# Optimization experiments

Measured on AMD Instinct MI355X. Metric: run time of the kernel, lower is better.

## Reference

```python
import jax, jax.numpy as jnp
import numpy as np

N, E = 100000, 1600000
D_IN, D_H, D_OUT = 128, 128, 64


def _lin(key, fan_in, fan_out):
    return jax.random.normal(key, (fan_out, fan_in), jnp.float32) / np.sqrt(fan_in).astype(np.float32)


def setup_inputs() -> dict:
    key = jax.random.key(0)
    ks = jax.random.split(key, 12)
    x = jax.random.normal(ks[0], (N, D_IN), jnp.float32)
    edge_index = jax.random.randint(ks[1], (2, E), 0, N, dtype=jnp.int64)
    inp = {
        "x": x,
        "edge_index": edge_index,
        "emb_W": _lin(ks[2], D_IN, D_H),
        "emb_b": jnp.zeros((D_H,), jnp.float32),
        # SAGEConv layer 0 (hidden -> hidden): lin_l (on aggregated msgs, with bias), lin_r (root, no bias)
        "Wl0": _lin(ks[3], D_H, D_H), "bl0": jnp.zeros((D_H,), jnp.float32), "Wr0": _lin(ks[4], D_H, D_H),
        # SAGEConv layer 1 (hidden -> hidden)
        "Wl1": _lin(ks[5], D_H, D_H), "bl1": jnp.zeros((D_H,), jnp.float32), "Wr1": _lin(ks[6], D_H, D_H),
        # SAGEConv layer 2 (hidden -> out)
        "Wl2": _lin(ks[7], D_H, D_OUT), "bl2": jnp.zeros((D_OUT,), jnp.float32), "Wr2": _lin(ks[8], D_H, D_OUT),
    }
    return inp


def _sage_conv(h, src, dst, Wl, bl, Wr):
    # mean aggregation of source-node messages at destination nodes
    msg = h[src]                                               # [E, H] gather
    agg = jax.ops.segment_sum(msg, dst, num_segments=N)        # [N, H]
    cnt = jax.ops.segment_sum(jnp.ones((src.shape[0], 1), h.dtype), dst, num_segments=N)
    mean = agg / jnp.maximum(cnt, 1.0)
    return mean @ Wl.T + bl + h @ Wr.T


def reference(x, edge_index, emb_W, emb_b, Wl0, bl0, Wr0, Wl1, bl1, Wr1, Wl2, bl2, Wr2):
    src, dst = edge_index[0], edge_index[1]
    h = x @ emb_W.T + emb_b                                    # node_embedding Linear
    h = jax.nn.relu(_sage_conv(h, src, dst, Wl0, bl0, Wr0))    # dropout = identity (eval)
    h = jax.nn.relu(_sage_conv(h, src, dst, Wl1, bl1, Wr1))
    h = _sage_conv(h, src, dst, Wl2, bl2, Wr2)                 # final layer: no relu/dropout
    return h
```

## Files before the change

### kernel.cpp

```cpp
#include <hip/hip_runtime.h>

typedef __attribute__((ext_vector_type(8))) short short8;
typedef __attribute__((ext_vector_type(4))) float f32x4;
typedef __attribute__((ext_vector_type(2))) float f32x2;

#define NODE_D 128
#define ECH 16384
#define PSH 9

__device__ __forceinline__ float bf2f(ushort u) {
    union { uint i; float f; } c; c.i = ((uint)u) << 16; return c.f;
}
__device__ __forceinline__ ushort f2bf(float f) {
    union { float f; uint i; } c; c.f = f;
    return (ushort)((c.i + 0x7FFF + ((c.i >> 16) & 1)) >> 16);
}
__device__ __forceinline__ uchar f2e4m3(float f) {
    uint w = (uint)__builtin_amdgcn_cvt_pk_fp8_f32(f, f, 0, false);
    return (uchar)(w & 0xff);
}

__global__ __launch_bounds__(256) void k_count(const int* __restrict__ dst,
                                               int* __restrict__ cm,
                                               int E, int NC,
                                               const float* __restrict__ s0, const float* __restrict__ s1,
                                               const float* __restrict__ s2, const float* __restrict__ s3,
                                               const float* __restrict__ s4, const float* __restrict__ s5,
                                               const float* __restrict__ s6, ushort* __restrict__ wdst) {
    if ((int)blockIdx.x >= NC) {
        int i = ((int)blockIdx.x - NC) * 256 + threadIdx.x;
        if (i >= 98304) return;
        const float* s; int off;
        if (i < 16384)      { s = s0; off = i; }
        else if (i < 32768) { s = s1; off = i - 16384; }
        else if (i < 49152) { s = s2; off = i - 32768; }
        else if (i < 65536) { s = s3; off = i - 49152; }
        else if (i < 81920) { s = s4; off = i - 65536; }
        else if (i < 90112) { s = s5; off = i - 81920; }
        else                { s = s6; off = i - 90112; }
        wdst[i] = f2bf(s[off]);
        return;
    }
    __shared__ int lh[256];
    lh[threadIdx.x] = 0;
    __syncthreads();
    int c = blockIdx.x;
    int lo = c * ECH, hi = min(lo + ECH, E);
    for (int i = lo + (int)threadIdx.x; i < hi; i += 256)
        atomicAdd(&lh[dst[i] >> PSH], 1);
    __syncthreads();
    cm[c * 256 + threadIdx.x] = lh[threadIdx.x];
}

__global__ __launch_bounds__(256) void k_pscan(const int* __restrict__ cm,
                                               int* __restrict__ om,
                                               int* __restrict__ pbase,
                                               int* __restrict__ rowptrN,
                                               int NC, int NP, int E) {
    __shared__ int ts[256];
    int p = threadIdx.x;
    int s = 0;
    if (p < NP)
        for (int c = 0; c < NC; ++c) s += cm[c * 256 + p];
    ts[p] = s;
    __syncthreads();
    for (int st = 1; st < 256; st <<= 1) {
        int add = (p >= st) ? ts[p - st] : 0;
        __syncthreads();
        ts[p] += add;
        __syncthreads();
    }
    int base = ts[p] - s;
    if (p < NP) {
        int run = base;
        for (int c = 0; c < NC; ++c) {
            om[c * 256 + p] = run;
            run += cm[c * 256 + p];
        }
        pbase[p] = base;
    }
    if (p == 0) { pbase[NP] = E; rowptrN[0] = E; }
}

__global__ __launch_bounds__(256) void k_scatter3(const int* __restrict__ src,
                                                  const int* __restrict__ dst,
                                                  const int* __restrict__ om,
                                                  uint* __restrict__ ebuf, int E) {
    __shared__ int cur[256];
    int c = blockIdx.x;
    cur[threadIdx.x] = om[c * 256 + threadIdx.x];
    __syncthreads();
    int lo = c * ECH, hi = min(lo + ECH, E);
    for (int i = lo + (int)threadIdx.x; i < hi; i += 256) {
        int d = dst[i];
        int pos = atomicAdd(&cur[d >> PSH], 1);
        ebuf[pos] = ((uint)(d & 511) << 17) | (uint)src[i];
    }
}

__global__ __launch_bounds__(256) void k_local(const uint* __restrict__ ebuf,
                                               const int* __restrict__ pbase,
                                               int* __restrict__ rowptr,
                                               int* __restrict__ col, int N) {
    __shared__ int hist[512];
    __shared__ int cur[512];
    __shared__ int ts[256];
    int p = blockIdx.x;
    int t = threadIdx.x;
    int lo = pbase[p], hi = pbase[p + 1];
    hist[t] = 0; hist[t + 256] = 0;
    __syncthreads();
    for (int j = lo + t; j < hi; j += 256)
        atomicAdd(&hist[ebuf[j] >> 17], 1);
    __syncthreads();
    int v0 = hist[2 * t], v1 = hist[2 * t + 1];
    int s = v0 + v1;
    ts[t] = s;
    __syncthreads();
    for (int st = 1; st < 256; st <<= 1) {
        int add = (t >= st) ? ts[t - st] : 0;
        __syncthreads();
        ts[t] += add;
        __syncthreads();
    }
    int excl = ts[t] - s + lo;
    int node0 = (p << PSH) + 2 * t;
    if (node0 < N) rowptr[node0] = excl;
    if (node0 + 1 < N) rowptr[node0 + 1] = excl + v0;
    cur[2 * t] = excl;
    cur[2 * t + 1] = excl + v0;
    __syncthreads();
    for (int j = lo + t; j < hi; j += 256) {
        uint e = ebuf[j];
        int pos = atomicAdd(&cur[e >> 17], 1);
        col[pos] = (int)(e & 0x1FFFF);
    }
}

__global__ __launch_bounds__(256) void k_aggf(const uchar* __restrict__ hq,
                                              const int* __restrict__ rowptr,
                                              const int* __restrict__ col,
                                              ushort* __restrict__ mean, int N) {
    int node = blockIdx.x * 4 + (threadIdx.x >> 6);
    if (node >= N) return;
    int lane = threadIdx.x & 63;
    int half = lane >> 5;
    int l32  = lane & 31;
    int beg = rowptr[node];
    int end = rowptr[node + 1];
    float inv = 1.f / fmaxf((float)(end - beg), 1.f);
    const uchar* base = hq + l32 * 4;
    float a0 = 0.f, a1 = 0.f, a2 = 0.f, a3 = 0.f;
    for (int jb0 = beg; jb0 < end; jb0 += 16) {
        int bj = jb0 + half * 8;
        uint v[8];
        float mk[8];
        #pragma unroll
        for (int q = 0; q < 8; ++q) {
            int j = bj + q;
            int s = col[j < end ? j : end - 1];
            v[q] = *(const uint*)(base + (size_t)s * 128);
            mk[q] = (j < end) ? 1.f : 0.f;
        }
        #pragma unroll
        for (int q = 0; q < 8; ++q) {
            f32x2 lo = __builtin_amdgcn_cvt_pk_f32_fp8(v[q], false);
            f32x2 hi = __builtin_amdgcn_cvt_pk_f32_fp8(v[q], true);
            a0 += mk[q] * lo[0]; a1 += mk[q] * lo[1];
            a2 += mk[q] * hi[0]; a3 += mk[q] * hi[1];
        }
    }
    a0 += __shfl_xor(a0, 32); a1 += __shfl_xor(a1, 32);
    a2 += __shfl_xor(a2, 32); a3 += __shfl_xor(a3, 32);
    if (half == 0) {
        uint2 o;
        o.x = (uint)f2bf(a0 * inv) | ((uint)f2bf(a1 * inv) << 16);
        o.y = (uint)f2bf(a2 * inv) | ((uint)f2bf(a3 * inv) << 16);
        *(uint2*)(mean + (size_t)node * 128 + l32 * 4) = o;
    }
}

template<int OD, bool DUAL, bool RELU, int OMODE, bool A0F32>
__global__ __launch_bounds__(256) void k_mm(const void* __restrict__ A0,
                                            const ushort* __restrict__ A1,
                                            const ushort* __restrict__ W0,
                                            const ushort* __restrict__ W1,
                                            const float* __restrict__ bias,
                                            void* __restrict__ outp,
                                            uchar* __restrict__ f8out, int N) {
    constexpr int NK    = DUAL ? 4 : 2;
    constexpr int M_REP = (OD == 128) ? 4 : 2;
    constexpr int N_REP = 4;
    constexpr int WROWS = M_REP * 16;

    __shared__ __align__(16) ushort sA[128 * 64];
    __shared__ __align__(16) ushort sW[OD * 64];

    const int t    = threadIdx.x;
    const int wid  = t >> 6;
    const int lane = t & 63;
    const int l15  = lane & 15;
    const int lhi  = lane >> 4;
    const int r0   = blockIdx.x * 128;

    int wm, wn0;
    if (OD == 128) { wm = wid >> 1; wn0 = (wid & 1) * 64; }
    else           { wm = wid;      wn0 = 0; }

    f32x4 zero = {0.f, 0.f, 0.f, 0.f};
    f32x4 acc[M_REP][N_REP];
    #pragma unroll
    for (int m = 0; m < M_REP; ++m)
        #pragma unroll
        for (int n = 0; n < N_REP; ++n) acc[m][n] = zero;

    const ushort* A0b = (const ushort*)A0;
    const float*  A0f = (const float*)A0;

    for (int kc = 0; kc < NK; ++kc) {
        const ushort* Ws = (DUAL && kc >= 2) ? W1 : W0;
        const ushort* As = (DUAL && kc >= 2) ? A1 : A0b;
        const int kloc = (kc & 1) * 64;

        __syncthreads();
        #pragma unroll
        for (int it = 0; it < 4; ++it) {
            int slot = it * 256 + t;
            int row = slot >> 3, k8 = slot & 7;
            int gr = r0 + row; if (gr >= N) gr = N - 1;
            short8 v;
            if (A0F32 && kc < 2) {
                float4 p = *(const float4*)(A0f + (size_t)gr * 128 + kloc + k8 * 8);
                float4 q = *(const float4*)(A0f + (size_t)gr * 128 + kloc + k8 * 8 + 4);
                v[0] = (short)f2bf(p.x); v[1] = (short)f2bf(p.y);
                v[2] = (short)f2bf(p.z); v[3] = (short)f2bf(p.w);
                v[4] = (short)f2bf(q.x); v[5] = (short)f2bf(q.y);
                v[6] = (short)f2bf(q.z); v[7] = (short)f2bf(q.w);
            } else {
                v = *(const short8*)(As + (size_t)gr * 128 + kloc + k8 * 8);
            }
            *(short8*)((char*)sA + ((row * 128 + k8 * 16) ^ ((row & 7) << 4))) = v;
        }
        #pragma unroll
        for (int it = 0; it < OD / 32; ++it) {
            int slot = it * 256 + t;
            int row = slot >> 3, k8 = slot & 7;
            short8 v = *(const short8*)(Ws + (size_t)row * 128 + kloc + k8 * 8);
            *(short8*)((char*)sW + ((row * 128 + k8 * 16) ^ ((row & 7) << 4))) = v;
        }
        __syncthreads();

        #pragma unroll
        for (int kb = 0; kb < 2; ++kb) {
            short8 af[M_REP], bfr[N_REP];
            #pragma unroll
            for (int m = 0; m < M_REP; ++m) {
                int row = wm * WROWS + m * 16 + l15;
                af[m] = *(const short8*)((const char*)sA +
                        ((row * 128 + kb * 64 + lhi * 16) ^ ((row & 7) << 4)));
            }
            #pragma unroll
            for (int n = 0; n < N_REP; ++n) {
                int colr = wn0 + n * 16 + l15;
                bfr[n] = *(const short8*)((const char*)sW +
                         ((colr * 128 + kb * 64 + lhi * 16) ^ ((colr & 7) << 4)));
            }
            #pragma unroll
            for (int m = 0; m < M_REP; ++m)
                #pragma unroll
                for (int n = 0; n < N_REP; ++n)
                    acc[m][n] = __builtin_amdgcn_mfma_f32_16x16x32_bf16(af[m], bfr[n], acc[m][n], 0, 0, 0);
        }
    }

    float bv[N_REP];
    #pragma unroll
    for (int n = 0; n < N_REP; ++n) bv[n] = bias ? bias[wn0 + n * 16 + l15] : 0.f;

    #pragma unroll
    for (int m = 0; m < M_REP; ++m) {
        #pragma unroll
        for (int r = 0; r < 4; ++r) {
            int grow = r0 + wm * WROWS + m * 16 + lhi * 4 + r;
            if (grow < N) {
                #pragma unroll
                for (int n = 0; n < N_REP; ++n) {
                    int colr = wn0 + n * 16 + l15;
                    float v = acc[m][n][r] + bv[n];
                    if (RELU) v = fmaxf(v, 0.f);
                    if constexpr (OMODE != 3)
                        ((ushort*)outp)[(size_t)grow * OD + colr] = f2bf(v);
                    if constexpr (OMODE == 2 || OMODE == 3)
                        f8out[(size_t)grow * OD + colr] = f2e4m3(v);
                }
            }
        }
    }
}

__global__ __launch_bounds__(256) void k_fin(const uchar* __restrict__ gq,
                                             const ushort* __restrict__ h_in,
                                             const ushort* __restrict__ W0,
                                             const float* __restrict__ bias,
                                             const int* __restrict__ rowptr,
                                             const int* __restrict__ col,
                                             float* __restrict__ outp, int N) {
    __shared__ __align__(16) ushort ga[128 * 64];
    __shared__ __align__(16) ushort sA[128 * 64];
    __shared__ __align__(16) ushort sW[64 * 64];

    const int t    = threadIdx.x;
    const int wid  = t >> 6;
    const int lane = t & 63;
    const int g    = lane >> 4;
    const int c16  = lane & 15;
    const int r0   = blockIdx.x * 128;

    for (int it = 0; it < 8; ++it) {
        int nl = it * 16 + wid * 4 + g;
        int node = r0 + nl;
        float a0 = 0.f, a1 = 0.f, a2 = 0.f, a3 = 0.f;
        if (node < N) {
            int beg = rowptr[node], end = rowptr[node + 1];
            float inv = 1.f / fmaxf((float)(end - beg), 1.f);
            const uchar* base = gq + c16 * 4;
            for (int jb0 = beg; jb0 < end; jb0 += 8) {
                uint v[8];
                float mk[8];
                #pragma unroll
                for (int q = 0; q < 8; ++q) {
                    int j = jb0 + q;
                    int s = col[j < end ? j : end - 1];
                    v[q] = *(const uint*)(base + (size_t)s * 64);
                    mk[q] = (j < end) ? 1.f : 0.f;
                }
                #pragma unroll
                for (int q = 0; q < 8; ++q) {
                    f32x2 lo = __builtin_amdgcn_cvt_pk_f32_fp8(v[q], false);
                    f32x2 hi = __builtin_amdgcn_cvt_pk_f32_fp8(v[q], true);
                    a0 += mk[q] * lo[0]; a1 += mk[q] * lo[1];
                    a2 += mk[q] * hi[0]; a3 += mk[q] * hi[1];
                }
            }
            a0 *= inv; a1 *= inv; a2 *= inv; a3 *= inv;
        }
        uint2 o;
        o.x = (uint)f2bf(a0) | ((uint)f2bf(a1) << 16);
        o.y = (uint)f2bf(a2) | ((uint)f2bf(a3) << 16);
        *(uint2*)((char*)ga + nl * 128 + c16 * 8) = o;
    }

    const int l15 = lane & 15;
    const int lhi = lane >> 4;

    f32x4 zero = {0.f, 0.f, 0.f, 0.f};
    f32x4 acc[2][4];
    #pragma unroll
    for (int m = 0; m < 2; ++m)
        #pragma unroll
        for (int n = 0; n < 4; ++n) acc[m][n] = zero;

    for (int kc = 0; kc < 2; ++kc) {
        const int kloc = kc * 64;
        __syncthreads();
        #pragma unroll
        for (int it = 0; it < 4; ++it) {
            int slot = it * 256 + t;
            int row = slot >> 3, k8 = slot & 7;
            int gr = r0 + row; if (gr >= N) gr = N - 1;
            short8 v = *(const short8*)(h_in + (size_t)gr * 128 + kloc + k8 * 8);
            *(short8*)((char*)sA + ((row * 128 + k8 * 16) ^ ((row & 7) << 4))) = v;
        }
        #pragma unroll
        for (int it = 0; it < 2; ++it) {
            int slot = it * 256 + t;
            int row = slot >> 3, k8 = slot & 7;
            short8 v = *(const short8*)(W0 + (size_t)row * 128 + kloc + k8 * 8);
            *(short8*)((char*)sW + ((row * 128 + k8 * 16) ^ ((row & 7) << 4))) = v;
        }
        __syncthreads();

        #pragma unroll
        for (int kb = 0; kb < 2; ++kb) {
            short8 af[2], bfr[4];
            #pragma unroll
            for (int m = 0; m < 2; ++m) {
                int row = wid * 32 + m * 16 + l15;
                af[m] = *(const short8*)((const char*)sA +
                        ((row * 128 + kb * 64 + lhi * 16) ^ ((row & 7) << 4)));
            }
            #pragma unroll
            for (int n = 0; n < 4; ++n) {
                int colr = n * 16 + l15;
                bfr[n] = *(const short8*)((const char*)sW +
                         ((colr * 128 + kb * 64 + lhi * 16) ^ ((colr & 7) << 4)));
            }
            #pragma unroll
            for (int m = 0; m < 2; ++m)
                #pragma unroll
                for (int n = 0; n < 4; ++n)
                    acc[m][n] = __builtin_amdgcn_mfma_f32_16x16x32_bf16(af[m], bfr[n], acc[m][n], 0, 0, 0);
        }
    }

    float bv[4];
    #pragma unroll
    for (int n = 0; n < 4; ++n) bv[n] = bias[n * 16 + l15];

    #pragma unroll
    for (int m = 0; m < 2; ++m) {
        #pragma unroll
        for (int r = 0; r < 4; ++r) {
            int rl = wid * 32 + m * 16 + lhi * 4 + r;
            int grow = r0 + rl;
            if (grow < N) {
                #pragma unroll
                for (int n = 0; n < 4; ++n) {
                    int colr = n * 16 + l15;
                    float v = acc[m][n][r] + bv[n] + bf2f(ga[rl * 64 + colr]);
                    outp[(size_t)grow * 64 + colr] = v;
                }
            }
        }
    }
}

extern "C" void kernel_launch(void* const* d_in, const int* in_sizes, int n_in,
                              void* d_out, int out_size, void* d_ws, size_t ws_size,
                              hipStream_t stream) {
    const float* x     = (const float*)d_in[0];
    const int*   eidx  = (const int*)d_in[1];
    const float* emb_W = (const float*)d_in[2];
    const float* emb_b = (const float*)d_in[3];
    const float* Wl0   = (const float*)d_in[4];
    const float* bl0   = (const float*)d_in[5];
    const float* Wr0   = (const float*)d_in[6];
    const float* Wl1   = (const float*)d_in[7];
    const float* bl1   = (const float*)d_in[8];
    const float* Wr1   = (const float*)d_in[9];
    const float* Wl2   = (const float*)d_in[10];
    const float* bl2   = (const float*)d_in[11];
    const float* Wr2   = (const float*)d_in[12];

    const int N = in_sizes[0] / NODE_D;
    const int E = in_sizes[1] / 2;
    const int* src = eidx;
    const int* dst = eidx + E;
    const int NC = (E + ECH - 1) / ECH;
    const int NP = (N + (1 << PSH) - 1) >> PSH;

    char* w = (char*)d_ws;
    ushort* h_bf    = (ushort*)w; w += (size_t)N * 128 * sizeof(ushort);
    ushort* mean_bf = (ushort*)w; w += (size_t)N * 128 * sizeof(ushort);
    ushort* wbf     = (ushort*)w; w += (size_t)98304 * sizeof(ushort);
    uchar* q8_a     = (uchar*)w;  w += (size_t)N * 128;
    uchar* q8_b     = (uchar*)w;  w += (size_t)N * 128;
    uint* ebuf      = (uint*)w;   w += (size_t)E * sizeof(uint);
    int* cm     = (int*)w; w += (size_t)NC * 256 * sizeof(int);
    int* om     = (int*)w; w += (size_t)NC * 256 * sizeof(int);
    int* pbase  = (int*)w; w += (size_t)(NP + 1) * sizeof(int);
    int* rowptr = (int*)w; w += (size_t)(N + 1) * sizeof(int);
    int* col    = (int*)w; w += (size_t)E * sizeof(int);

    uchar* g2_q8 = (uchar*)mean_bf;

    const ushort* embB = wbf;
    const ushort* Wl0B = wbf + 16384;
    const ushort* Wr0B = wbf + 32768;
    const ushort* Wl1B = wbf + 49152;
    const ushort* Wr1B = wbf + 65536;
    const ushort* Wl2B = wbf + 81920;
    const ushort* Wr2B = wbf + 90112;

    const int TPB = 256;

    hipLaunchKernelGGL(k_count, dim3(NC + 384), dim3(TPB), 0, stream,
                       dst, cm, E, NC, emb_W, Wl0, Wr0, Wl1, Wr1, Wl2, Wr2, wbf);
    hipLaunchKernelGGL(k_pscan, dim3(1), dim3(TPB), 0, stream,
                       cm, om, pbase, rowptr + N, NC, NP, E);
    hipLaunchKernelGGL(k_scatter3, dim3(NC), dim3(TPB), 0, stream, src, dst, om, ebuf, E);
    hipLaunchKernelGGL(k_local, dim3(NP), dim3(TPB), 0, stream, ebuf, pbase, rowptr, col, N);

    const int dgrid = (N + 127) / 128;
    const int agrid = (N + 3) / 4;

    hipLaunchKernelGGL((k_mm<128, false, false, 2, true>), dim3(dgrid), dim3(TPB), 0, stream,
                       (const void*)x, (const ushort*)nullptr, embB, (const ushort*)nullptr,
                       emb_b, h_bf, q8_a, N);

    hipLaunchKernelGGL(k_aggf, dim3(agrid), dim3(TPB), 0, stream, q8_a, rowptr, col, mean_bf, N);
    hipLaunchKernelGGL((k_mm<128, true, true, 2, false>), dim3(dgrid), dim3(TPB), 0, stream,
                       (const void*)mean_bf, h_bf, Wl0B, Wr0B, bl0, h_bf, q8_b, N);

    hipLaunchKernelGGL(k_aggf, dim3(agrid), dim3(TPB), 0, stream, q8_b, rowptr, col, mean_bf, N);
    hipLaunchKernelGGL((k_mm<128, true, true, 0, false>), dim3(dgrid), dim3(TPB), 0, stream,
                       (const void*)mean_bf, h_bf, Wl1B, Wr1B, bl1, h_bf, (uchar*)nullptr, N);

    hipLaunchKernelGGL((k_mm<64, false, false, 3, false>), dim3(dgrid), dim3(TPB), 0, stream,
                       (const void*)h_bf, (const ushort*)nullptr, Wl2B, (const ushort*)nullptr,
                       (const float*)nullptr, (void*)nullptr, g2_q8, N);
    hipLaunchKernelGGL(k_fin, dim3(dgrid), dim3(TPB), 0, stream,
                       g2_q8, h_bf, Wr2B, bl2, rowptr, col, (float*)d_out, N);
}
```

Before: 305.9 us.

## Widen aggregation gathers to 8-byte loads and shrink edge chunk size

The hidden-layer aggregation kernel now has each lane load 8 fp8 bytes per neighbor with 16 lanes per row, so four neighbor groups are processed per wavefront and reduced with two xor shuffles into a single 16-byte store. Both aggregation loops use packed f32x2 accumulation instead of staging values in arrays, which cuts register pressure. The edge-chunk size used by the CSR build drops from 16384 to 4096, creating more blocks for the counting and scatter phases. The trade-offs are more shuffle work, fewer neighbors in flight per lane, and more per-chunk overhead in the CSR build.

```diff
diff --git a/kernel.cpp b/kernel.cpp
--- a/kernel.cpp
+++ b/kernel.cpp
@@ -5,7 +5,7 @@
 typedef __attribute__((ext_vector_type(2))) float f32x2;
 
 #define NODE_D 128
-#define ECH 16384
+#define ECH 4096
 #define PSH 9
 
 __device__ __forceinline__ float bf2f(ushort u) {
@@ -144,39 +144,40 @@
     int node = blockIdx.x * 4 + (threadIdx.x >> 6);
     if (node >= N) return;
     int lane = threadIdx.x & 63;
-    int half = lane >> 5;
-    int l32  = lane & 31;
+    int grp  = lane >> 4;
+    int l16  = lane & 15;
     int beg = rowptr[node];
     int end = rowptr[node + 1];
     float inv = 1.f / fmaxf((float)(end - beg), 1.f);
-    const uchar* base = hq + l32 * 4;
-    float a0 = 0.f, a1 = 0.f, a2 = 0.f, a3 = 0.f;
-    for (int jb0 = beg; jb0 < end; jb0 += 16) {
-        int bj = jb0 + half * 8;
-        uint v[8];
-        float mk[8];
-        #pragma unroll
-        for (int q = 0; q < 8; ++q) {
-            int j = bj + q;
+    const uchar* base = hq + l16 * 8;
+    f32x2 a01 = {0.f, 0.f}, a23 = {0.f, 0.f}, a45 = {0.f, 0.f}, a67 = {0.f, 0.f};
+    for (int jb0 = beg; jb0 < end; jb0 += 8) {
+        #pragma unroll
+        for (int q = 0; q < 2; ++q) {
+            int j = jb0 + grp * 2 + q;
             int s = col[j < end ? j : end - 1];
-            v[q] = *(const uint*)(base + (size_t)s * 128);
-            mk[q] = (j < end) ? 1.f : 0.f;
-        }
-        #pragma unroll
-        for (int q = 0; q < 8; ++q) {
-            f32x2 lo = __builtin_amdgcn_cvt_pk_f32_fp8(v[q], false);
-            f32x2 hi = __builtin_amdgcn_cvt_pk_f32_fp8(v[q], true);
-            a0 += mk[q] * lo[0]; a1 += mk[q] * lo[1];
-            a2 += mk[q] * hi[0]; a3 += mk[q] * hi[1];
-        }
-    }
-    a0 += __shfl_xor(a0, 32); a1 += __shfl_xor(a1, 32);
-    a2 += __shfl_xor(a2, 32); a3 += __shfl_xor(a3, 32);
-    if (half == 0) {
-        uint2 o;
-        o.x = (uint)f2bf(a0 * inv) | ((uint)f2bf(a1 * inv) << 16);
-        o.y = (uint)f2bf(a2 * inv) | ((uint)f2bf(a3 * inv) << 16);
-        *(uint2*)(mean + (size_t)node * 128 + l32 * 4) = o;
+            uint2 v = *(const uint2*)(base + (size_t)s * 128);
+            float m = (j < end) ? 1.f : 0.f;
+            f32x2 mk = {m, m};
+            a01 += mk * __builtin_amdgcn_cvt_pk_f32_fp8(v.x, false);
+            a23 += mk * __builtin_amdgcn_cvt_pk_f32_fp8(v.x, true);
+            a45 += mk * __builtin_amdgcn_cvt_pk_f32_fp8(v.y, false);
+            a67 += mk * __builtin_amdgcn_cvt_pk_f32_fp8(v.y, true);
+        }
+    }
+    float r[8] = {a01[0], a01[1], a23[0], a23[1], a45[0], a45[1], a67[0], a67[1]};
+    #pragma unroll
+    for (int i = 0; i < 8; ++i) {
+        r[i] += __shfl_xor(r[i], 16);
+        r[i] += __shfl_xor(r[i], 32);
+    }
+    if (lane < 16) {
+        uint4 o;
+        o.x = (uint)f2bf(r[0] * inv) | ((uint)f2bf(r[1] * inv) << 16);
+        o.y = (uint)f2bf(r[2] * inv) | ((uint)f2bf(r[3] * inv) << 16);
+        o.z = (uint)f2bf(r[4] * inv) | ((uint)f2bf(r[5] * inv) << 16);
+        o.w = (uint)f2bf(r[6] * inv) | ((uint)f2bf(r[7] * inv) << 16);
+        *(uint4*)(mean + (size_t)node * 128 + l16 * 8) = o;
     }
 }
 
@@ -319,34 +320,28 @@
     for (int it = 0; it < 8; ++it) {
         int nl = it * 16 + wid * 4 + g;
         int node = r0 + nl;
-        float a0 = 0.f, a1 = 0.f, a2 = 0.f, a3 = 0.f;
+        f32x2 a01 = {0.f, 0.f}, a23 = {0.f, 0.f};
+        float inv = 1.f;
         if (node < N) {
             int beg = rowptr[node], end = rowptr[node + 1];
-            float inv = 1.f / fmaxf((float)(end - beg), 1.f);
+            inv = 1.f / fmaxf((float)(end - beg), 1.f);
             const uchar* base = gq + c16 * 4;
             for (int jb0 = beg; jb0 < end; jb0 += 8) {
-                uint v[8];
-                float mk[8];
                 #pragma unroll
                 for (int q = 0; q < 8; ++q) {
                     int j = jb0 + q;
                     int s = col[j < end ? j : end - 1];
-                    v[q] = *(const uint*)(base + (size_t)s * 64);
-                    mk[q] = (j < end) ? 1.f : 0.f;
+                    uint v = *(const uint*)(base + (size_t)s * 64);
+                    float m = (j < end) ? 1.f : 0.f;
+                    f32x2 mk = {m, m};
+                    a01 += mk * __builtin_amdgcn_cvt_pk_f32_fp8(v, false);
+                    a23 += mk * __builtin_amdgcn_cvt_pk_f32_fp8(v, true);
                 }
-                #pragma unroll
-                for (int q = 0; q < 8; ++q) {
-                    f32x2 lo = __builtin_amdgcn_cvt_pk_f32_fp8(v[q], false);
-                    f32x2 hi = __builtin_amdgcn_cvt_pk_f32_fp8(v[q], true);
-                    a0 += mk[q] * lo[0]; a1 += mk[q] * lo[1];
-                    a2 += mk[q] * hi[0]; a3 += mk[q] * hi[1];
-                }
-            }
-            a0 *= inv; a1 *= inv; a2 *= inv; a3 *= inv;
+            }
         }
         uint2 o;
-        o.x = (uint)f2bf(a0) | ((uint)f2bf(a1) << 16);
-        o.y = (uint)f2bf(a2) | ((uint)f2bf(a3) << 16);
+        o.x = (uint)f2bf(a01[0] * inv) | ((uint)f2bf(a01[1] * inv) << 16);
+        o.y = (uint)f2bf(a23[0] * inv) | ((uint)f2bf(a23[1] * inv) << 16);
         *(uint2*)((char*)ga + nl * 128 + c16 * 8) = o;
     }
 
```

Result: slower. 337.9 us (+10.5%).
